# Kernel tuning notes

Measured on AMD Instinct MI355X. Metric: run time of the kernel, lower is better.

Reference implementation:

```python
import jax, jax.numpy as jnp
import numpy as np

EMBED_DIM = 256
SEQ_LEN = 4096
BATCH = 8
ALPHA = 0.99


def setup_inputs() -> dict:
    key = jax.random.key(0)
    k_x, k_w, k_b = jax.random.split(key, 3)
    x = jax.random.normal(k_x, (BATCH, SEQ_LEN, EMBED_DIM), dtype=jnp.float32)
    # nn.Linear(embed_dim, 3*embed_dim): store as [d, 3d] so y = x @ Wqkv + bqkv
    Wqkv = jax.random.normal(k_w, (EMBED_DIM, 3 * EMBED_DIM), dtype=jnp.float32) * (EMBED_DIM ** -0.5)
    bqkv = jax.random.normal(k_b, (3 * EMBED_DIM,), dtype=jnp.float32) * 0.02
    return {"x": x, "Wqkv": Wqkv, "bqkv": bqkv}


def reference(x, Wqkv, bqkv):
    bs, sl, d = x.shape
    qkv = x @ Wqkv + bqkv                      # [bs, sl, 3d]
    q, k, v = jnp.split(qkv, 3, axis=-1)       # each [bs, sl, d]
    # causal * exponential-decay mask: M[i, j] = alpha**(i-j) for j <= i else 0
    i = jnp.arange(sl, dtype=jnp.float32)
    M = jnp.where(i[:, None] >= i[None, :],
                  jnp.power(jnp.float32(ALPHA), i[:, None] - i[None, :]),
                  0.0)                          # [sl, sl]
    scores = jnp.einsum('bqd,bkd->bqk', q, k) / jnp.sqrt(jnp.float32(d))
    out = jnp.einsum('bqk,bkd->bqd', scores * M, v)
    return out
```

## Files before the change

### kernel.cpp

```cpp
#include <hip/hip_runtime.h>

typedef __bf16 bf16x8 __attribute__((ext_vector_type(8)));
typedef float f32x4 __attribute__((ext_vector_type(4)));
typedef unsigned short u16;
typedef unsigned int u32;
typedef u16 u16x4 __attribute__((ext_vector_type(4)));
typedef u16 u16x8 __attribute__((ext_vector_type(8)));

#define L2ALPHA (-0.014499569f)

static __device__ __forceinline__ u16 f2bf(float f) {
    u32 u = __builtin_bit_cast(u32, f);
    return (u16)((u + 0x7FFFu + ((u >> 16) & 1u)) >> 16);
}

static __device__ __forceinline__ void gl2lds16(const void* g, void* l) {
    __builtin_amdgcn_global_load_lds(
        (const __attribute__((address_space(1))) u32*)g,
        (__attribute__((address_space(3))) u32*)l, 16, 0, 0);
}

__global__ __launch_bounds__(256, 2) void proj_kernel(
        const float* __restrict__ x, const float* __restrict__ Wq,
        const float* __restrict__ bias,
        u16* __restrict__ qb, u16* __restrict__ kb, u16* __restrict__ vb)
{
    __shared__ __align__(16) u16 Bs[32 * 128 * 8];
    __shared__ __align__(16) u16 As[4][32 * 40];

    const int tid = threadIdx.x, lane = tid & 63, w = tid >> 6;
    const int l = blockIdx.x;
    const int nb = l % 6;
    const int mt = l / 6;
    const int m0 = mt * 128, n0 = nb * 128;
    const int m = lane & 15, quad = lane >> 4;

    {
        const int col = tid & 127;
        const int khalf = tid >> 7;
        #pragma unroll
        for (int s = 0; s < 32; ++s) {
            int k0 = (khalf + 2 * s) * 4;
            u16x4 h;
            #pragma unroll
            for (int i = 0; i < 4; ++i)
                h[i] = f2bf(Wq[(k0 + i) * 768 + n0 + col]);
            *(u16x4*)&Bs[((k0 >> 3) * 128 + col) * 8 + (k0 & 7)] = h;
        }
    }
    __syncthreads();

    const int r = lane & 31, h = lane >> 5;
    const float* xrow = x + (size_t)(m0 + w * 32 + r) * 256 + h * 16;
    u16* As_w = &As[w][0];

    f32x4 acc[2][8];
    #pragma unroll
    for (int rt = 0; rt < 2; ++rt)
        #pragma unroll
        for (int ct = 0; ct < 8; ++ct)
            acc[rt][ct] = f32x4{0.f, 0.f, 0.f, 0.f};

    float4 g0 = *(const float4*)(xrow + 0);
    float4 g1 = *(const float4*)(xrow + 4);
    float4 g2 = *(const float4*)(xrow + 8);
    float4 g3 = *(const float4*)(xrow + 12);

    for (int kt = 0; kt < 8; ++kt) {
        u16x8 ha, hb;
        ha[0]=f2bf(g0.x); ha[1]=f2bf(g0.y); ha[2]=f2bf(g0.z); ha[3]=f2bf(g0.w);
        ha[4]=f2bf(g1.x); ha[5]=f2bf(g1.y); ha[6]=f2bf(g1.z); ha[7]=f2bf(g1.w);
        hb[0]=f2bf(g2.x); hb[1]=f2bf(g2.y); hb[2]=f2bf(g2.z); hb[3]=f2bf(g2.w);
        hb[4]=f2bf(g3.x); hb[5]=f2bf(g3.y); hb[6]=f2bf(g3.z); hb[7]=f2bf(g3.w);
        *(u16x8*)&As_w[r * 40 + h * 16]     = ha;
        *(u16x8*)&As_w[r * 40 + h * 16 + 8] = hb;

        if (kt < 7) {
            const float* xn = xrow + (kt + 1) * 32;
            g0 = *(const float4*)(xn + 0);
            g1 = *(const float4*)(xn + 4);
            g2 = *(const float4*)(xn + 8);
            g3 = *(const float4*)(xn + 12);
        }

        asm volatile("s_waitcnt lgkmcnt(0)" ::: "memory");

        bf16x8 af[2], bfr[8];
        #pragma unroll
        for (int rt = 0; rt < 2; ++rt)
            af[rt] = *(const bf16x8*)&As_w[(rt * 16 + m) * 40 + quad * 8];
        #pragma unroll
        for (int ct = 0; ct < 8; ++ct)
            bfr[ct] = *(const bf16x8*)&Bs[((kt * 4 + quad) * 128 + ct * 16 + m) * 8];
        #pragma unroll
        for (int rt = 0; rt < 2; ++rt)
            #pragma unroll
            for (int ct = 0; ct < 8; ++ct)
                acc[rt][ct] = __builtin_amdgcn_mfma_f32_16x16x32_bf16(
                    af[rt], bfr[ct], acc[rt][ct], 0, 0, 0);
    }

    const int b = m0 >> 12;
    const int jbase = (m0 & 4095) + w * 32;
    const int d0 = (nb & 1) * 128;

    if (nb < 2) {
        #pragma unroll
        for (int rt = 0; rt < 2; ++rt)
            #pragma unroll
            for (int ct = 0; ct < 8; ++ct) {
                int coll = ct * 16 + m;
                float bv = bias[d0 + coll];
                #pragma unroll
                for (int rr = 0; rr < 4; ++rr) {
                    int row = m0 + w * 32 + rt * 16 + quad * 4 + rr;
                    qb[(size_t)row * 256 + d0 + coll] = f2bf((acc[rt][ct][rr] + bv) * 0.0625f);
                }
            }
    } else if (nb < 4) {
        #pragma unroll
        for (int rt = 0; rt < 2; ++rt)
            #pragma unroll
            for (int ct = 0; ct < 8; ++ct) {
                int d = d0 + ct * 16 + m;
                float bv = bias[256 + d];
                int k8 = d >> 5, qk = (d >> 3) & 3, e = d & 7;
                #pragma unroll
                for (int rr = 0; rr < 4; ++rr) {
                    int j = jbase + rt * 16 + quad * 4 + rr;
                    int jt = j >> 5, jj = j & 31;
                    kb[((((size_t)(b * 128 + jt) * 2 + (jj & 1)) * 8 + k8) * 64 + qk * 16 + (jj >> 1)) * 8 + e]
                        = f2bf(acc[rt][ct][rr] + bv);
                }
            }
    } else {
        #pragma unroll
        for (int rt = 0; rt < 2; ++rt)
            #pragma unroll
            for (int ct = 0; ct < 8; ++ct) {
                int d = d0 + ct * 16 + m;
                float bv = bias[512 + d];
                int dt = d >> 4, mv = d & 15;
                int j = jbase + rt * 16 + quad * 4;
                int jt = j >> 5, qv = (j >> 3) & 3, e0 = j & 7;
                u16x4 hv;
                #pragma unroll
                for (int rr = 0; rr < 4; ++rr) hv[rr] = f2bf(acc[rt][ct][rr] + bv);
                *(u16x4*)&vb[(((size_t)(b * 128 + jt) * 16 + dt) * 64 + qv * 16 + mv) * 8 + e0] = hv;
            }
    }
}

__global__ __launch_bounds__(512, 2) void attn_kernel(
        const u16* __restrict__ qb, const u16* __restrict__ kb,
        const u16* __restrict__ vb, float* __restrict__ out)
{
    __shared__ __align__(16) u16 KV[2][2][16384];
    __shared__ __align__(16) u16 Ps[8 * 32 * 40];

    const int tid = threadIdx.x, lane = tid & 63, w = tid >> 6;
    const int wp = w & 3, par = w >> 2;
    const int l = blockIdx.x;
    const int b = l & 7;
    const int m0 = (l >> 3) * 128;
    const int qrow0 = m0 + wp * 32;
    const int m = lane & 15, quad = lane >> 4;
    const size_t rowbase = (size_t)b * 4096;
    const size_t pbase = (size_t)b * 128;

    bf16x8 qf[2][8];
    #pragma unroll
    for (int rg = 0; rg < 2; ++rg)
        #pragma unroll
        for (int k8 = 0; k8 < 8; ++k8)
            qf[rg][k8] = *(const bf16x8*)(qb + (rowbase + qrow0 + rg * 16 + m) * 256 + k8 * 32 + quad * 8);

    f32x4 acc[2][16];
    #pragma unroll
    for (int rg = 0; rg < 2; ++rg)
        #pragma unroll
        for (int dt = 0; dt < 16; ++dt)
            acc[rg][dt] = f32x4{0.f, 0.f, 0.f, 0.f};

    int t0 = (m0 - 1024) >> 5; if (t0 < 0) t0 = 0;
    const int t1 = (m0 >> 5) + 3;
    const int nIter = (t1 - t0 + 2) >> 1;

    {
        const u16* kpA = kb + (pbase + t0) * 8192;
        const u16* vpA = vb + (pbase + t0) * 8192;
        const u16* kpB = kpA + 8192;
        const u16* vpB = vpA + 8192;
        #pragma unroll
        for (int s = 0; s < 2; ++s) {
            int c = tid + 512 * s;
            gl2lds16(kpA + (size_t)c * 8, &KV[0][0][c * 8]);
            gl2lds16(vpA + (size_t)c * 8, &KV[0][0][8192 + c * 8]);
            gl2lds16(kpB + (size_t)c * 8, &KV[0][1][c * 8]);
            gl2lds16(vpB + (size_t)c * 8, &KV[0][1][8192 + c * 8]);
        }
    }

    int p = 0;
    for (int it = 0; it < nIter; ++it) {
        __syncthreads();
        if (it + 1 < nIter) {
            const int ta = t0 + 2 * (it + 1);
            const bool haveB = (ta + 1 <= t1);
            const u16* kpA = kb + (pbase + ta) * 8192;
            const u16* vpA = vb + (pbase + ta) * 8192;
            #pragma unroll
            for (int s = 0; s < 2; ++s) {
                int c = tid + 512 * s;
                gl2lds16(kpA + (size_t)c * 8, &KV[p ^ 1][0][c * 8]);
                gl2lds16(vpA + (size_t)c * 8, &KV[p ^ 1][0][8192 + c * 8]);
                if (haveB) {
                    gl2lds16(kpA + 8192 + (size_t)c * 8, &KV[p ^ 1][1][c * 8]);
                    gl2lds16(vpA + 8192 + (size_t)c * 8, &KV[p ^ 1][1][8192 + c * 8]);
                }
            }
        }

        const int t = t0 + 2 * it + par;
        const int j0 = t * 32;
        if (t <= t1 && j0 <= qrow0 + 31 && j0 + 1055 >= qrow0) {
            const u16* Kt = &KV[p][par][0];
            const u16* Vt = &KV[p][par][8192];

            f32x4 sA0{0.f,0.f,0.f,0.f}, sA1{0.f,0.f,0.f,0.f};
            f32x4 sB0{0.f,0.f,0.f,0.f}, sB1{0.f,0.f,0.f,0.f};
            #pragma unroll
            for (int k8 = 0; k8 < 8; ++k8) {
                bf16x8 bf0 = *(const bf16x8*)&Kt[(k8 * 64 + lane) * 8];
                sA0 = __builtin_amdgcn_mfma_f32_16x16x32_bf16(qf[0][k8], bf0, sA0, 0, 0, 0);
                sA1 = __builtin_amdgcn_mfma_f32_16x16x32_bf16(qf[1][k8], bf0, sA1, 0, 0, 0);
            }
            #pragma unroll
            for (int k8 = 0; k8 < 8; ++k8) {
                bf16x8 bf1 = *(const bf16x8*)&Kt[((8 + k8) * 64 + lane) * 8];
                sB0 = __builtin_amdgcn_mfma_f32_16x16x32_bf16(qf[0][k8], bf1, sB0, 0, 0, 0);
                sB1 = __builtin_amdgcn_mfma_f32_16x16x32_bf16(qf[1][k8], bf1, sB1, 0, 0, 0);
            }

            #pragma unroll
            for (int rg = 0; rg < 2; ++rg) {
                f32x4 sh0 = rg ? sA1 : sA0;
                f32x4 sh1 = rg ? sB1 : sB0;
                #pragma unroll
                for (int rr = 0; rr < 4; ++rr) {
                    int i = qrow0 + rg * 16 + quad * 4 + rr;
                    int dd0 = i - (j0 + 2 * m);
                    int dd1 = dd0 - 1;
                    float w0 = (dd0 >= 0) ? __builtin_amdgcn_exp2f((float)dd0 * L2ALPHA) : 0.0f;
                    float w1 = (dd1 >= 0) ? __builtin_amdgcn_exp2f((float)dd1 * L2ALPHA) : 0.0f;
                    int rowb = (w * 32 + rg * 16 + quad * 4 + rr) * 40;
                    u32 pv = (u32)f2bf(sh0[rr] * w0) | ((u32)f2bf(sh1[rr] * w1) << 16);
                    *(u32*)&Ps[rowb + 2 * m] = pv;
                }
            }
            asm volatile("s_waitcnt lgkmcnt(0)" ::: "memory");

            bf16x8 pa0 = *(const bf16x8*)&Ps[(w * 32 + m) * 40 + quad * 8];
            bf16x8 pa1 = *(const bf16x8*)&Ps[(w * 32 + 16 + m) * 40 + quad * 8];

            #pragma unroll
            for (int dt = 0; dt < 16; ++dt) {
                bf16x8 vf = *(const bf16x8*)&Vt[(dt * 64 + lane) * 8];
                acc[0][dt] = __builtin_amdgcn_mfma_f32_16x16x32_bf16(pa0, vf, acc[0][dt], 0, 0, 0);
                acc[1][dt] = __builtin_amdgcn_mfma_f32_16x16x32_bf16(pa1, vf, acc[1][dt], 0, 0, 0);
            }
        }
        p ^= 1;
    }

    __syncthreads();
    float* Comb = (float*)&KV[0][0][0];
    if (par == 1) {
        float* dst = Comb + (size_t)wp * 8192 + lane * 128;
        #pragma unroll
        for (int rg = 0; rg < 2; ++rg)
            #pragma unroll
            for (int dt = 0; dt < 16; ++dt)
                *(f32x4*)(dst + (rg * 16 + dt) * 4) = acc[rg][dt];
    }
    __syncthreads();
    if (par == 0) {
        const float* src = Comb + (size_t)wp * 8192 + lane * 128;
        #pragma unroll
        for (int rg = 0; rg < 2; ++rg)
            #pragma unroll
            for (int dt = 0; dt < 16; ++dt) {
                f32x4 o = acc[rg][dt] + *(const f32x4*)(src + (rg * 16 + dt) * 4);
                #pragma unroll
                for (int rr = 0; rr < 4; ++rr)
                    out[(rowbase + qrow0 + rg * 16 + quad * 4 + rr) * 256 + dt * 16 + m] = o[rr];
            }
    }
}

extern "C" void kernel_launch(void* const* d_in, const int* in_sizes, int n_in,
                              void* d_out, int out_size, void* d_ws, size_t ws_size,
                              hipStream_t stream) {
    (void)in_sizes; (void)n_in; (void)out_size; (void)ws_size;
    const float* x    = (const float*)d_in[0];
    const float* Wq   = (const float*)d_in[1];
    const float* bias = (const float*)d_in[2];
    float* outp = (float*)d_out;

    const size_t per = (size_t)8 * 4096 * 256;
    u16* qb = (u16*)d_ws;
    u16* kb = qb + per;
    u16* vb = kb + per;

    proj_kernel<<<1536, 256, 0, stream>>>(x, Wq, bias, qb, kb, vb);
    attn_kernel<<<256, 512, 0, stream>>>(qb, kb, vb, outp);
}
```

Baseline: 177.8 us.

## Persist projection blocks over four row tiles and load x fragments directly

The projection kernel now launches 384 blocks, each converting its W column slice to bf16 in LDS once and reusing it across four 128-row tiles, instead of 1536 blocks that each redo the W conversion. The A operand is now loaded straight from global memory into MFMA fragments, which drops the LDS staging buffer and its wait. The attention kernel's cross-wave combine buffer switches to a lane-contiguous layout to reduce LDS bank conflicts. The risks are fewer blocks for latency hiding and unstaged, less coalesced global loads of x.

```diff
diff --git a/kernel.cpp b/kernel.cpp
--- a/kernel.cpp
+++ b/kernel.cpp
@@ -26,13 +26,12 @@
         u16* __restrict__ qb, u16* __restrict__ kb, u16* __restrict__ vb)
 {
     __shared__ __align__(16) u16 Bs[32 * 128 * 8];
-    __shared__ __align__(16) u16 As[4][32 * 40];
 
     const int tid = threadIdx.x, lane = tid & 63, w = tid >> 6;
     const int l = blockIdx.x;
-    const int nb = l % 6;
-    const int mt = l / 6;
-    const int m0 = mt * 128, n0 = nb * 128;
+    const int nb = l >> 6;
+    const int chunk = l & 63;
+    const int n0 = nb * 128;
     const int m = lane & 15, quad = lane >> 4;
 
     {
@@ -50,104 +49,92 @@
     }
     __syncthreads();
 
-    const int r = lane & 31, h = lane >> 5;
-    const float* xrow = x + (size_t)(m0 + w * 32 + r) * 256 + h * 16;
-    u16* As_w = &As[w][0];
-
-    f32x4 acc[2][8];
-    #pragma unroll
-    for (int rt = 0; rt < 2; ++rt)
-        #pragma unroll
-        for (int ct = 0; ct < 8; ++ct)
-            acc[rt][ct] = f32x4{0.f, 0.f, 0.f, 0.f};
-
-    float4 g0 = *(const float4*)(xrow + 0);
-    float4 g1 = *(const float4*)(xrow + 4);
-    float4 g2 = *(const float4*)(xrow + 8);
-    float4 g3 = *(const float4*)(xrow + 12);
-
-    for (int kt = 0; kt < 8; ++kt) {
-        u16x8 ha, hb;
-        ha[0]=f2bf(g0.x); ha[1]=f2bf(g0.y); ha[2]=f2bf(g0.z); ha[3]=f2bf(g0.w);
-        ha[4]=f2bf(g1.x); ha[5]=f2bf(g1.y); ha[6]=f2bf(g1.z); ha[7]=f2bf(g1.w);
-        hb[0]=f2bf(g2.x); hb[1]=f2bf(g2.y); hb[2]=f2bf(g2.z); hb[3]=f2bf(g2.w);
-        hb[4]=f2bf(g3.x); hb[5]=f2bf(g3.y); hb[6]=f2bf(g3.z); hb[7]=f2bf(g3.w);
-        *(u16x8*)&As_w[r * 40 + h * 16]     = ha;
-        *(u16x8*)&As_w[r * 40 + h * 16 + 8] = hb;
-
-        if (kt < 7) {
-            const float* xn = xrow + (kt + 1) * 32;
-            g0 = *(const float4*)(xn + 0);
-            g1 = *(const float4*)(xn + 4);
-            g2 = *(const float4*)(xn + 8);
-            g3 = *(const float4*)(xn + 12);
-        }
-
-        asm volatile("s_waitcnt lgkmcnt(0)" ::: "memory");
-
-        bf16x8 af[2], bfr[8];
+    const int b_d0 = (nb & 1) * 128;
+
+    for (int it = 0; it < 4; ++it) {
+        const int m0 = (chunk * 4 + it) * 128;
+        const float* xw = x + (size_t)(m0 + w * 32 + m) * 256 + quad * 8;
+
+        f32x4 acc[2][8];
         #pragma unroll
         for (int rt = 0; rt < 2; ++rt)
-            af[rt] = *(const bf16x8*)&As_w[(rt * 16 + m) * 40 + quad * 8];
-        #pragma unroll
-        for (int ct = 0; ct < 8; ++ct)
-            bfr[ct] = *(const bf16x8*)&Bs[((kt * 4 + quad) * 128 + ct * 16 + m) * 8];
-        #pragma unroll
-        for (int rt = 0; rt < 2; ++rt)
             #pragma unroll
             for (int ct = 0; ct < 8; ++ct)
-                acc[rt][ct] = __builtin_amdgcn_mfma_f32_16x16x32_bf16(
-                    af[rt], bfr[ct], acc[rt][ct], 0, 0, 0);
-    }
-
-    const int b = m0 >> 12;
-    const int jbase = (m0 & 4095) + w * 32;
-    const int d0 = (nb & 1) * 128;
-
-    if (nb < 2) {
-        #pragma unroll
-        for (int rt = 0; rt < 2; ++rt)
-            #pragma unroll
-            for (int ct = 0; ct < 8; ++ct) {
-                int coll = ct * 16 + m;
-                float bv = bias[d0 + coll];
-                #pragma unroll
-                for (int rr = 0; rr < 4; ++rr) {
-                    int row = m0 + w * 32 + rt * 16 + quad * 4 + rr;
-                    qb[(size_t)row * 256 + d0 + coll] = f2bf((acc[rt][ct][rr] + bv) * 0.0625f);
-                }
-            }
-    } else if (nb < 4) {
-        #pragma unroll
-        for (int rt = 0; rt < 2; ++rt)
-            #pragma unroll
-            for (int ct = 0; ct < 8; ++ct) {
-                int d = d0 + ct * 16 + m;
-                float bv = bias[256 + d];
-                int k8 = d >> 5, qk = (d >> 3) & 3, e = d & 7;
-                #pragma unroll
-                for (int rr = 0; rr < 4; ++rr) {
-                    int j = jbase + rt * 16 + quad * 4 + rr;
-                    int jt = j >> 5, jj = j & 31;
-                    kb[((((size_t)(b * 128 + jt) * 2 + (jj & 1)) * 8 + k8) * 64 + qk * 16 + (jj >> 1)) * 8 + e]
-                        = f2bf(acc[rt][ct][rr] + bv);
-                }
-            }
-    } else {
-        #pragma unroll
-        for (int rt = 0; rt < 2; ++rt)
-            #pragma unroll
-            for (int ct = 0; ct < 8; ++ct) {
-                int d = d0 + ct * 16 + m;
-                float bv = bias[512 + d];
-                int dt = d >> 4, mv = d & 15;
-                int j = jbase + rt * 16 + quad * 4;
-                int jt = j >> 5, qv = (j >> 3) & 3, e0 = j & 7;
-                u16x4 hv;
-                #pragma unroll
-                for (int rr = 0; rr < 4; ++rr) hv[rr] = f2bf(acc[rt][ct][rr] + bv);
-                *(u16x4*)&vb[(((size_t)(b * 128 + jt) * 16 + dt) * 64 + qv * 16 + mv) * 8 + e0] = hv;
-            }
+                acc[rt][ct] = f32x4{0.f, 0.f, 0.f, 0.f};
+
+        #pragma unroll
+        for (int kt = 0; kt < 8; ++kt) {
+            bf16x8 af[2];
+            #pragma unroll
+            for (int rt = 0; rt < 2; ++rt) {
+                const float* xp = xw + (size_t)rt * 16 * 256 + kt * 32;
+                float4 a0 = *(const float4*)(xp);
+                float4 a1 = *(const float4*)(xp + 4);
+                u16x8 h;
+                h[0]=f2bf(a0.x); h[1]=f2bf(a0.y); h[2]=f2bf(a0.z); h[3]=f2bf(a0.w);
+                h[4]=f2bf(a1.x); h[5]=f2bf(a1.y); h[6]=f2bf(a1.z); h[7]=f2bf(a1.w);
+                af[rt] = __builtin_bit_cast(bf16x8, h);
+            }
+            bf16x8 bfr[8];
+            #pragma unroll
+            for (int ct = 0; ct < 8; ++ct)
+                bfr[ct] = *(const bf16x8*)&Bs[((kt * 4 + quad) * 128 + ct * 16 + m) * 8];
+            #pragma unroll
+            for (int rt = 0; rt < 2; ++rt)
+                #pragma unroll
+                for (int ct = 0; ct < 8; ++ct)
+                    acc[rt][ct] = __builtin_amdgcn_mfma_f32_16x16x32_bf16(
+                        af[rt], bfr[ct], acc[rt][ct], 0, 0, 0);
+        }
+
+        const int b = m0 >> 12;
+        const int jbase = (m0 & 4095) + w * 32;
+
+        if (nb < 2) {
+            #pragma unroll
+            for (int rt = 0; rt < 2; ++rt)
+                #pragma unroll
+                for (int ct = 0; ct < 8; ++ct) {
+                    int coll = ct * 16 + m;
+                    float bv = bias[b_d0 + coll];
+                    #pragma unroll
+                    for (int rr = 0; rr < 4; ++rr) {
+                        int row = m0 + w * 32 + rt * 16 + quad * 4 + rr;
+                        qb[(size_t)row * 256 + b_d0 + coll] = f2bf((acc[rt][ct][rr] + bv) * 0.0625f);
+                    }
+                }
+        } else if (nb < 4) {
+            #pragma unroll
+            for (int rt = 0; rt < 2; ++rt)
+                #pragma unroll
+                for (int ct = 0; ct < 8; ++ct) {
+                    int d = b_d0 + ct * 16 + m;
+                    float bv = bias[256 + d];
+                    int k8 = d >> 5, qk = (d >> 3) & 3, e = d & 7;
+                    #pragma unroll
+                    for (int rr = 0; rr < 4; ++rr) {
+                        int j = jbase + rt * 16 + quad * 4 + rr;
+                        int jt = j >> 5, jj = j & 31;
+                        kb[((((size_t)(b * 128 + jt) * 2 + (jj & 1)) * 8 + k8) * 64 + qk * 16 + (jj >> 1)) * 8 + e]
+                            = f2bf(acc[rt][ct][rr] + bv);
+                    }
+                }
+        } else {
+            #pragma unroll
+            for (int rt = 0; rt < 2; ++rt)
+                #pragma unroll
+                for (int ct = 0; ct < 8; ++ct) {
+                    int d = b_d0 + ct * 16 + m;
+                    float bv = bias[512 + d];
+                    int dt = d >> 4, mv = d & 15;
+                    int j = jbase + rt * 16 + quad * 4;
+                    int jt = j >> 5, qv = (j >> 3) & 3, e0 = j & 7;
+                    u16x4 hv;
+                    #pragma unroll
+                    for (int rr = 0; rr < 4; ++rr) hv[rr] = f2bf(acc[rt][ct][rr] + bv);
+                    *(u16x4*)&vb[(((size_t)(b * 128 + jt) * 16 + dt) * 64 + qv * 16 + mv) * 8 + e0] = hv;
+                }
+        }
     }
 }
 
@@ -189,15 +176,13 @@
     {
         const u16* kpA = kb + (pbase + t0) * 8192;
         const u16* vpA = vb + (pbase + t0) * 8192;
-        const u16* kpB = kpA + 8192;
-        const u16* vpB = vpA + 8192;
         #pragma unroll
         for (int s = 0; s < 2; ++s) {
             int c = tid + 512 * s;
             gl2lds16(kpA + (size_t)c * 8, &KV[0][0][c * 8]);
             gl2lds16(vpA + (size_t)c * 8, &KV[0][0][8192 + c * 8]);
-            gl2lds16(kpB + (size_t)c * 8, &KV[0][1][c * 8]);
-            gl2lds16(vpB + (size_t)c * 8, &KV[0][1][8192 + c * 8]);
+            gl2lds16(kpA + 8192 + (size_t)c * 8, &KV[0][1][c * 8]);
+            gl2lds16(vpA + 8192 + (size_t)c * 8, &KV[0][1][8192 + c * 8]);
         }
     }
 
@@ -276,21 +261,21 @@
     __syncthreads();
     float* Comb = (float*)&KV[0][0][0];
     if (par == 1) {
-        float* dst = Comb + (size_t)wp * 8192 + lane * 128;
+        float* dst = Comb + ((size_t)wp * 32 * 64 + lane) * 4;
         #pragma unroll
         for (int rg = 0; rg < 2; ++rg)
             #pragma unroll
             for (int dt = 0; dt < 16; ++dt)
-                *(f32x4*)(dst + (rg * 16 + dt) * 4) = acc[rg][dt];
+                *(f32x4*)(dst + (rg * 16 + dt) * 256) = acc[rg][dt];
     }
     __syncthreads();
     if (par == 0) {
-        const float* src = Comb + (size_t)wp * 8192 + lane * 128;
+        const float* src = Comb + ((size_t)wp * 32 * 64 + lane) * 4;
         #pragma unroll
         for (int rg = 0; rg < 2; ++rg)
             #pragma unroll
             for (int dt = 0; dt < 16; ++dt) {
-                f32x4 o = acc[rg][dt] + *(const f32x4*)(src + (rg * 16 + dt) * 4);
+                f32x4 o = acc[rg][dt] + *(const f32x4*)(src + (rg * 16 + dt) * 256);
                 #pragma unroll
                 for (int rr = 0; rr < 4; ++rr)
                     out[(rowbase + qrow0 + rg * 16 + quad * 4 + rr) * 256 + dt * 16 + m] = o[rr];
@@ -312,6 +297,6 @@
     u16* kb = qb + per;
     u16* vb = kb + per;
 
-    proj_kernel<<<1536, 256, 0, stream>>>(x, Wq, bias, qb, kb, vb);
+    proj_kernel<<<384, 256, 0, stream>>>(x, Wq, bias, qb, kb, vb);
     attn_kernel<<<256, 512, 0, stream>>>(qb, kb, vb, outp);
 }
```

Result: slower. 182.0 us (+2.4%).
